# Performance work log

Hardware: AMD Instinct MI355X
Metric: run time of the kernel (lower is better)

The kernel has to match this reference:

```python
import jax, jax.numpy as jnp
import numpy as np
from jax.scipy.special import logsumexp

B, T = 64, 1024
NF, NH = 512, 512
NK = 500          # n_kcs (chains)
NS = 2            # n_states == n_outputs == 2


def setup_inputs() -> dict:
    key = jax.random.key(0)
    ks = jax.random.split(key, 8)
    return {
        "corr": jax.random.randint(ks[0], (B, T), 0, 2),
        "kc": jax.random.randint(ks[1], (B, T), 0, NK),
        "FM": jax.random.normal(ks[2], (B, T, NF), dtype=jnp.float32),
        "W1": jax.random.normal(ks[3], (NF, NH), jnp.float32) / np.sqrt(NF).astype(np.float32),
        "b1": jnp.zeros((NH,), jnp.float32),
        "W2": jax.random.normal(ks[4], (NH, 2), jnp.float32) / np.sqrt(NH).astype(np.float32),
        "b2": jnp.zeros((2,), jnp.float32),
        "trans_logits": jax.random.normal(ks[5], (NK, NS, NS), jnp.float32),
        "obs_logits": jax.random.normal(ks[6], (NK, NS, 2), jnp.float32),
        "init_logits": jax.random.normal(ks[7], (NK, NS), jnp.float32),
    }


def _bkt_forward(corr, kc, FM, W1, b1, W2, b2, trans_logits, obs_logits, init_logits):
    # MLP producing per-timestep observation logit features
    h = jnp.tanh(FM @ W1 + b1)                 # [B,T,NH]
    o = h @ W2 + b2                            # [B,T,2] (one per state)
    fv = jnp.stack([o, -o], axis=3)            # [B,T,NS,2] == cat((o, -o), dim=3)

    n_batch = corr.shape[0]
    bidx = jnp.arange(n_batch)
    log_t = jax.nn.log_softmax(trans_logits, axis=1)          # [NK,NS,NS], softmax over dim 1
    la0 = jnp.tile(jax.nn.log_softmax(init_logits, axis=1)[None], (n_batch, 1, 1))  # [B,NK,NS]

    def step(la_all, xs):
        y, c, fv_t = xs                         # y:[B] obs, c:[B] chain, fv_t:[B,NS,2]
        log_obs = jax.nn.log_softmax(obs_logits[c] + fv_t, axis=2)   # [B,NS,2]
        la = la_all[bidx, c]                    # [B,NS] gather current chain alpha
        log_py = logsumexp(log_obs + la[:, :, None], axis=1)         # [B,2]
        log_py = log_py - logsumexp(log_py, axis=1, keepdims=True)
        # emission prob of observed symbol per state: log_obs[b,:,y[b]]
        lp = jnp.take_along_axis(log_obs, y[:, None, None], axis=2)[..., 0]  # [B,NS]
        new_la = logsumexp(lp[:, None, :] + la[:, None, :] + log_t[c], axis=2)  # [B,NS]
        la_all = la_all.at[bidx, c].set(new_la)
        return la_all, log_py

    xs = (corr.T, kc.T, jnp.moveaxis(fv, 1, 0))   # time-major for scan
    _, outs = jax.lax.scan(step, la0, xs)         # outs: [T,B,2]
    return jnp.transpose(outs, (1, 0, 2))         # [B,T,2]


def reference(corr, kc, FM, W1, b1, W2, b2, trans_logits, obs_logits, init_logits):
    return _bkt_forward(corr, kc, FM, W1, b1, W2, b2, trans_logits, obs_logits, init_logits)
```

## Files before the change

### kernel.cpp

```cpp
#include <hip/hip_runtime.h>
#include <hip/hip_bf16.h>
#include <stdint.h>

typedef unsigned short u16;
typedef __bf16 bf16x8 __attribute__((ext_vector_type(8)));
typedef float floatx4 __attribute__((ext_vector_type(4)));

#define B_SZ 64
#define T_SZ 1024
#define NK 500

__device__ __forceinline__ u16 f2bf(float f) {
    union { float f; uint32_t u; } v; v.f = f;
    uint32_t u = v.u;
    u += 0x7FFFu + ((u >> 16) & 1u);
    return (u16)(u >> 16);
}

__device__ __forceinline__ float exp2_hw(float x) { return __builtin_amdgcn_exp2f(x); }
__device__ __forceinline__ float log2_hw(float x) { return __builtin_amdgcn_logf(x); }

__device__ __forceinline__ float lse2(float a, float b) {
    float m = fmaxf(a, b);
    float d = fabsf(a - b);
    return fmaf(0.6931471805599453f,
                log2_hw(1.0f + exp2_hw(-d * 1.4426950408889634f)), m);
}

__global__ __launch_bounds__(256) void pack_w1(const float* __restrict__ in,
                                               u16* __restrict__ out) {
    int idx = blockIdx.x * 256 + threadIdx.x;
    int l     = idx & 63;
    int ks    = (idx >> 6) & 15;
    int ntile = idx >> 10;
    int col = l & 15, gg = l >> 4;
    int n = ntile * 16 + col;
    int kbase = ks * 32 + gg * 8;
    union { uint4 v; u16 s[8]; } p;
#pragma unroll
    for (int j = 0; j < 8; ++j)
        p.s[j] = f2bf(in[(size_t)(kbase + j) * 512 + n]);
    *(uint4*)(out + (size_t)idx * 8) = p.v;
}

__global__ __launch_bounds__(512, 4) void mlp_fused(
    const float* __restrict__ FM, const u16* __restrict__ W1P,
    const float* __restrict__ b1, const float* __restrict__ W2,
    const float* __restrict__ b2, float* __restrict__ o_buf) {

    __shared__ __align__(16) u16 ldsA[64 * 512];
    __shared__ float ldsO[64][8][2];

    const int tid  = threadIdx.x;
    const int w    = tid >> 6;
    const int lane = tid & 63;
    const int col  = lane & 15;
    const int g    = lane >> 4;
    const size_t row0 = (size_t)blockIdx.x * 64;

#pragma unroll
    for (int i = 0; i < 8; ++i) {
        int flat = i * 512 + tid;
        int row  = flat >> 6;
        int k8   = flat & 63;
        const float* src = FM + (row0 + row) * 512 + k8 * 8;
        float4 f0 = ((const float4*)src)[0];
        float4 f1 = ((const float4*)src)[1];
        union { uint4 v; u16 s[8]; } p;
        p.s[0] = f2bf(f0.x); p.s[1] = f2bf(f0.y);
        p.s[2] = f2bf(f0.z); p.s[3] = f2bf(f0.w);
        p.s[4] = f2bf(f1.x); p.s[5] = f2bf(f1.y);
        p.s[6] = f2bf(f1.z); p.s[7] = f2bf(f1.w);
        int sw = k8 ^ (row & 7);
        *(uint4*)(ldsA + row * 512 + sw * 8) = p.v;
    }
    __syncthreads();

    const u16* bbase = W1P + ((size_t)(w * 64) * 64 + lane) * 8;

    floatx4 acc[4][4];
    floatx4 zero = {0.f, 0.f, 0.f, 0.f};
#pragma unroll
    for (int mi = 0; mi < 4; mi++)
#pragma unroll
        for (int ni = 0; ni < 4; ni++) acc[mi][ni] = zero;

    bf16x8 bA[4], bB[4];
#pragma unroll
    for (int ni = 0; ni < 4; ni++)
        bA[ni] = *(const bf16x8*)(bbase + (ni * 16 + 0) * 512);

    for (int ks2 = 0; ks2 < 16; ks2 += 2) {
#pragma unroll
        for (int ni = 0; ni < 4; ni++)
            bB[ni] = *(const bf16x8*)(bbase + (ni * 16 + ks2 + 1) * 512);
        {
            bf16x8 afr[4];
            int sw = (ks2 * 4 + g) ^ (col & 7);
#pragma unroll
            for (int mi = 0; mi < 4; mi++)
                afr[mi] = *(const bf16x8*)(ldsA + (mi * 16 + col) * 512 + sw * 8);
#pragma unroll
            for (int mi = 0; mi < 4; mi++)
#pragma unroll
                for (int ni = 0; ni < 4; ni++)
                    acc[mi][ni] = __builtin_amdgcn_mfma_f32_16x16x32_bf16(
                        afr[mi], bA[ni], acc[mi][ni], 0, 0, 0);
        }
        int ksn = (ks2 + 2) & 15;
#pragma unroll
        for (int ni = 0; ni < 4; ni++)
            bA[ni] = *(const bf16x8*)(bbase + (ni * 16 + ksn) * 512);
        {
            bf16x8 afr[4];
            int sw = ((ks2 + 1) * 4 + g) ^ (col & 7);
#pragma unroll
            for (int mi = 0; mi < 4; mi++)
                afr[mi] = *(const bf16x8*)(ldsA + (mi * 16 + col) * 512 + sw * 8);
#pragma unroll
            for (int mi = 0; mi < 4; mi++)
#pragma unroll
                for (int ni = 0; ni < 4; ni++)
                    acc[mi][ni] = __builtin_amdgcn_mfma_f32_16x16x32_bf16(
                        afr[mi], bB[ni], acc[mi][ni], 0, 0, 0);
        }
    }

    float po[4][4][2];
#pragma unroll
    for (int mi = 0; mi < 4; mi++)
#pragma unroll
        for (int r = 0; r < 4; r++) { po[mi][r][0] = 0.f; po[mi][r][1] = 0.f; }

#pragma unroll
    for (int ni = 0; ni < 4; ni++) {
        int n = w * 64 + ni * 16 + col;
        float b1f = b1[n];
        float w20 = W2[2 * n], w21 = W2[2 * n + 1];
#pragma unroll
        for (int mi = 0; mi < 4; mi++)
#pragma unroll
            for (int r = 0; r < 4; r++) {
                float x = acc[mi][ni][r] + b1f;
                float ax = fabsf(x);
                float e = exp2_hw(-2.885390082f * ax);
                float t = (1.f - e) / (1.f + e);
                float h = copysignf(t, x);
                po[mi][r][0] += h * w20;
                po[mi][r][1] += h * w21;
            }
    }

#pragma unroll
    for (int mi = 0; mi < 4; mi++)
#pragma unroll
        for (int r = 0; r < 4; r++)
#pragma unroll
            for (int j = 0; j < 2; j++) {
                float v = po[mi][r][j];
                v += __shfl_xor(v, 1, 64);
                v += __shfl_xor(v, 2, 64);
                v += __shfl_xor(v, 4, 64);
                v += __shfl_xor(v, 8, 64);
                po[mi][r][j] = v;
            }
    if (col == 0) {
#pragma unroll
        for (int mi = 0; mi < 4; mi++)
#pragma unroll
            for (int r = 0; r < 4; r++) {
                int row = mi * 16 + g * 4 + r;
                ldsO[row][w][0] = po[mi][r][0];
                ldsO[row][w][1] = po[mi][r][1];
            }
    }
    __syncthreads();
    if (tid < 128) {
        int row = tid >> 1, j = tid & 1;
        float v = ldsO[row][0][j] + ldsO[row][1][j]
                + ldsO[row][2][j] + ldsO[row][3][j]
                + ldsO[row][4][j] + ldsO[row][5][j]
                + ldsO[row][6][j] + ldsO[row][7][j] + b2[j];
        o_buf[(row0 + row) * 2 + j] = v;
    }
}

__global__ __launch_bounds__(64) void bkt_scan(
    const int* __restrict__ corr, const int* __restrict__ kc,
    const float* __restrict__ trans_logits,
    const float* __restrict__ obs_logits,
    const float* __restrict__ init_logits,
    const float* __restrict__ o_buf,
    float* __restrict__ out) {

    __shared__ int s_kc[T_SZ];
    __shared__ int s_corr[T_SZ];
    __shared__ float2 s_o[T_SZ];
    const int b = blockIdx.x >> 3;
    const int g = blockIdx.x & 7;
    const int lane = threadIdx.x;

#pragma unroll
    for (int i = 0; i < 4; ++i) {
        int t4 = i * 64 + lane;
        ((int4*)s_kc)[t4]   = ((const int4*)(kc + b * T_SZ))[t4];
        ((int4*)s_corr)[t4] = ((const int4*)(corr + b * T_SZ))[t4];
    }
#pragma unroll
    for (int i = 0; i < 8; ++i) {
        int t4 = i * 64 + lane;
        ((float4*)s_o)[t4] = ((const float4*)(o_buf + (size_t)b * T_SZ * 2))[t4];
    }
    __syncthreads();

    const int c  = g * 64 + lane;
    const int cp = c < NK ? c : NK - 1;

    float ob00 = obs_logits[cp * 4 + 0], ob01 = obs_logits[cp * 4 + 1];
    float ob10 = obs_logits[cp * 4 + 2], ob11 = obs_logits[cp * 4 + 3];
    float tr00 = trans_logits[cp * 4 + 0], tr01 = trans_logits[cp * 4 + 1];
    float tr10 = trans_logits[cp * 4 + 2], tr11 = trans_logits[cp * 4 + 3];
    float n0 = lse2(tr00, tr10), n1 = lse2(tr01, tr11);
    float lt00 = tr00 - n0, lt01 = tr01 - n1;
    float lt10 = tr10 - n0, lt11 = tr11 - n1;
    float i0 = init_logits[cp * 2], i1 = init_logits[cp * 2 + 1];
    float nli = lse2(i0, i1);
    float la0 = i0 - nli, la1 = i1 - nli;

    for (int w16 = 0; w16 < 16; ++w16) {
        int tl = w16 * 64 + lane;
        unsigned long long mask = __ballot((s_kc[tl] >> 6) == g);
        while (mask) {
            int tz = __builtin_ctzll(mask);
            mask &= mask - 1;
            int t = w16 * 64 + tz;
            int kct = s_kc[t];
            if (c == kct) {
                float o0 = s_o[t].x, o1 = s_o[t].y;
                float x00 = ob00 + o0, x01 = ob01 - o0;
                float x10 = ob10 + o1, x11 = ob11 - o1;
                float d0 = lse2(x00, x01), d1 = lse2(x10, x11);
                float lo00 = x00 - d0, lo01 = x01 - d0;
                float lo10 = x10 - d1, lo11 = x11 - d1;
                float py0 = lse2(lo00 + la0, lo10 + la1);
                float py1 = lse2(lo01 + la0, lo11 + la1);
                float pn = lse2(py0, py1);
                ((float2*)out)[(size_t)b * T_SZ + t] = make_float2(py0 - pn, py1 - pn);
                float lp0 = s_corr[t] ? lo01 : lo00;
                float lp1 = s_corr[t] ? lo11 : lo10;
                float t0 = lp0 + la0, t1 = lp1 + la1;
                float nla0 = lse2(t0 + lt00, t1 + lt01);
                float nla1 = lse2(t0 + lt10, t1 + lt11);
                la0 = nla0; la1 = nla1;
            }
        }
    }
}

extern "C" void kernel_launch(void* const* d_in, const int* in_sizes, int n_in,
                              void* d_out, int out_size, void* d_ws, size_t ws_size,
                              hipStream_t stream) {
    const int*   corr = (const int*)d_in[0];
    const int*   kc   = (const int*)d_in[1];
    const float* FM   = (const float*)d_in[2];
    const float* W1   = (const float*)d_in[3];
    const float* b1   = (const float*)d_in[4];
    const float* W2   = (const float*)d_in[5];
    const float* b2   = (const float*)d_in[6];
    const float* trans_logits = (const float*)d_in[7];
    const float* obs_logits   = (const float*)d_in[8];
    const float* init_logits  = (const float*)d_in[9];
    float* out = (float*)d_out;

    u16*   w1p   = (u16*)d_ws;
    float* o_buf = (float*)((char*)d_ws + 512 * 512 * 2);

    pack_w1<<<128, 256, 0, stream>>>(W1, w1p);
    mlp_fused<<<1024, 512, 0, stream>>>(FM, w1p, b1, W2, b2, o_buf);
    bkt_scan<<<B_SZ * 8, 64, 0, stream>>>(corr, kc, trans_logits, obs_logits,
                                          init_logits, o_buf, out);
}
```

Measured before the change: 336.8 us.

## Stage W1 tiles through LDS via async global_load_lds double buffering

Per-wave W1 fragments now move through a double-buffered LDS region using global_load_lds direct loads, replacing register-prefetched global loads. Each block starts at a different K offset (blockIdx & 15) so blocks do not all hit the same W1 slice at once. Occupancy is lowered to 2 blocks per CU to make room for the extra 64KB of LDS, and manual waitcnt plus sched_barrier calls control the pipeline. Each wave only reads the slots it staged itself, so no block-wide sync is added, but the lower occupancy may cost latency hiding.

```diff
diff --git a/kernel.cpp b/kernel.cpp
--- a/kernel.cpp
+++ b/kernel.cpp
@@ -25,6 +25,13 @@
     float d = fabsf(a - b);
     return fmaf(0.6931471805599453f,
                 log2_hw(1.0f + exp2_hw(-d * 1.4426950408889634f)), m);
+}
+
+__device__ __forceinline__ void gload_lds16(const u16* g, u16* l) {
+    __builtin_amdgcn_global_load_lds(
+        (const __attribute__((address_space(1))) unsigned int*)g,
+        (__attribute__((address_space(3))) unsigned int*)l,
+        16, 0, 0);
 }
 
 __global__ __launch_bounds__(256) void pack_w1(const float* __restrict__ in,
@@ -43,12 +50,13 @@
     *(uint4*)(out + (size_t)idx * 8) = p.v;
 }
 
-__global__ __launch_bounds__(512, 4) void mlp_fused(
+__global__ __launch_bounds__(512, 2) void mlp_fused(
     const float* __restrict__ FM, const u16* __restrict__ W1P,
     const float* __restrict__ b1, const float* __restrict__ W2,
     const float* __restrict__ b2, float* __restrict__ o_buf) {
 
     __shared__ __align__(16) u16 ldsA[64 * 512];
+    __shared__ __align__(16) u16 ldsB[2][32 * 512];
     __shared__ float ldsO[64][8][2];
 
     const int tid  = threadIdx.x;
@@ -57,6 +65,7 @@
     const int col  = lane & 15;
     const int g    = lane >> 4;
     const size_t row0 = (size_t)blockIdx.x * 64;
+    const int kb = blockIdx.x & 15;
 
 #pragma unroll
     for (int i = 0; i < 8; ++i) {
@@ -76,7 +85,8 @@
     }
     __syncthreads();
 
-    const u16* bbase = W1P + ((size_t)(w * 64) * 64 + lane) * 8;
+    const u16* wbase = W1P + (size_t)(w * 4) * 16 * 512 + lane * 8;
+    u16* lb[2] = { &ldsB[0][(w * 4) * 512], &ldsB[1][(w * 4) * 512] };
 
     floatx4 acc[4][4];
     floatx4 zero = {0.f, 0.f, 0.f, 0.f};
@@ -85,46 +95,46 @@
 #pragma unroll
         for (int ni = 0; ni < 4; ni++) acc[mi][ni] = zero;
 
-    bf16x8 bA[4], bB[4];
-#pragma unroll
-    for (int ni = 0; ni < 4; ni++)
-        bA[ni] = *(const bf16x8*)(bbase + (ni * 16 + 0) * 512);
-
-    for (int ks2 = 0; ks2 < 16; ks2 += 2) {
+#define STAGEB(LB, KV) do {                                        \
+        const u16* gp_ = wbase + (size_t)(KV) * 512;               \
+        gload_lds16(gp_ + 0 * 16 * 512, (LB) + 0 * 512);           \
+        gload_lds16(gp_ + 1 * 16 * 512, (LB) + 1 * 512);           \
+        gload_lds16(gp_ + 2 * 16 * 512, (LB) + 2 * 512);           \
+        gload_lds16(gp_ + 3 * 16 * 512, (LB) + 3 * 512);           \
+    } while (0)
+
+    STAGEB(lb[0], kb);
+    STAGEB(lb[1], (kb + 1) & 15);
+
+#pragma unroll
+    for (int t = 0; t < 16; ++t) {
+        u16* cur = lb[t & 1];
+        if (t < 15) { asm volatile("s_waitcnt vmcnt(4)" ::: "memory"); }
+        else        { asm volatile("s_waitcnt vmcnt(0)" ::: "memory"); }
+        __builtin_amdgcn_sched_barrier(0);
+
+        int kv = (t + kb) & 15;
+        bf16x8 bB[4], afr[4];
 #pragma unroll
         for (int ni = 0; ni < 4; ni++)
-            bB[ni] = *(const bf16x8*)(bbase + (ni * 16 + ks2 + 1) * 512);
-        {
-            bf16x8 afr[4];
-            int sw = (ks2 * 4 + g) ^ (col & 7);
-#pragma unroll
-            for (int mi = 0; mi < 4; mi++)
-                afr[mi] = *(const bf16x8*)(ldsA + (mi * 16 + col) * 512 + sw * 8);
-#pragma unroll
-            for (int mi = 0; mi < 4; mi++)
-#pragma unroll
-                for (int ni = 0; ni < 4; ni++)
-                    acc[mi][ni] = __builtin_amdgcn_mfma_f32_16x16x32_bf16(
-                        afr[mi], bA[ni], acc[mi][ni], 0, 0, 0);
-        }
-        int ksn = (ks2 + 2) & 15;
-#pragma unroll
-        for (int ni = 0; ni < 4; ni++)
-            bA[ni] = *(const bf16x8*)(bbase + (ni * 16 + ksn) * 512);
-        {
-            bf16x8 afr[4];
-            int sw = ((ks2 + 1) * 4 + g) ^ (col & 7);
-#pragma unroll
-            for (int mi = 0; mi < 4; mi++)
-                afr[mi] = *(const bf16x8*)(ldsA + (mi * 16 + col) * 512 + sw * 8);
-#pragma unroll
-            for (int mi = 0; mi < 4; mi++)
-#pragma unroll
-                for (int ni = 0; ni < 4; ni++)
-                    acc[mi][ni] = __builtin_amdgcn_mfma_f32_16x16x32_bf16(
-                        afr[mi], bB[ni], acc[mi][ni], 0, 0, 0);
-        }
-    }
+            bB[ni] = *(const bf16x8*)(cur + ni * 512 + lane * 8);
+        int sw = (kv * 4 + g) ^ (col & 7);
+#pragma unroll
+        for (int mi = 0; mi < 4; mi++)
+            afr[mi] = *(const bf16x8*)(ldsA + (mi * 16 + col) * 512 + sw * 8);
+
+        asm volatile("s_waitcnt lgkmcnt(0)" ::: "memory");
+        __builtin_amdgcn_sched_barrier(0);
+        if (t < 14) STAGEB(cur, (t + 2 + kb) & 15);
+
+#pragma unroll
+        for (int mi = 0; mi < 4; mi++)
+#pragma unroll
+            for (int ni = 0; ni < 4; ni++)
+                acc[mi][ni] = __builtin_amdgcn_mfma_f32_16x16x32_bf16(
+                    afr[mi], bB[ni], acc[mi][ni], 0, 0, 0);
+    }
+#undef STAGEB
 
     float po[4][4][2];
 #pragma unroll
```

New measurement: 304.6 us. -9.6%, faster.
